# Performance work log

Measured on AMD Instinct MI355X. Metric: run time of the kernel, lower is better.

## Reference

```python
import jax, jax.numpy as jnp
import numpy as np

NSAMPLE = 32
LAMBDA = 0.5


def setup_inputs() -> dict:
    key = jax.random.key(0)
    k1, k2, k3, k4, k5 = jax.random.split(key, 5)
    B, N, NPOINT, C, NCOMP = 4, 8192, 2048, 64, 16
    xyz = jax.random.normal(k1, (B, N, 3), dtype=jnp.float32)
    new_xyz = jax.random.normal(k2, (B, NPOINT, 3), dtype=jnp.float32)
    components = jax.random.randint(k3, (B, N, 1), 0, NCOMP, dtype=jnp.int64)
    new_components = jax.random.randint(k4, (B, NPOINT, 1), 0, NCOMP, dtype=jnp.int64)
    features = jax.random.normal(k5, (B, C, N), dtype=jnp.float32)
    return {"xyz": xyz, "new_xyz": new_xyz, "components": components,
            "new_components": new_components, "features": features}


def _gag_knn(new_xyz, xyz, new_comp, comp, k, lam):
    # squared pairwise distances (B, npoint, N), same math as sum((src-dst)**2)
    diff = new_xyz[:, :, None, :] - xyz[:, None, :, :]
    dists = jnp.sum(diff * diff, axis=-1)
    # component-aware rescale
    mask = comp[:, None, :] == new_comp[:, :, None]  # (B, npoint, N)
    dists = jnp.where(mask, dists * lam, dists * (1.0 - lam))
    # full argsort then take first k (faithful to original)
    idx = jnp.argsort(dists, axis=-1)[:, :, :k]  # (B, npoint, k)
    return idx.astype(jnp.int32)


def reference(xyz, new_xyz, components, new_components, features):
    comp = components[..., 0]
    new_comp = new_components[..., 0]
    idx = _gag_knn(new_xyz, xyz, new_comp, comp, NSAMPLE, LAMBDA)  # (B, npoint, ns)

    # group xyz: gather along N -> (B, npoint, ns, 3)
    grouped_xyz = jnp.take_along_axis(xyz[:, None, :, :], idx[..., None], axis=2)
    grouped_xyz = grouped_xyz - new_xyz[:, :, None, :]
    grouped_xyz = jnp.transpose(grouped_xyz, (0, 3, 1, 2))  # (B, 3, npoint, ns)

    # group features: (B, C, N) -> (B, npoint, ns, C) -> (B, C, npoint, ns)
    feats_bnc = jnp.transpose(features, (0, 2, 1))  # (B, N, C)
    grouped_feats = jnp.take_along_axis(feats_bnc[:, None, :, :], idx[..., None], axis=2)
    grouped_feats = jnp.transpose(grouped_feats, (0, 3, 1, 2))  # (B, C, npoint, ns)

    return jnp.concatenate([grouped_xyz, grouped_feats], axis=1)  # (B, 3+C, npoint, ns)
```

## Files before the change

kernel.cpp:

```cpp
#include <hip/hip_runtime.h>


#define BQ 4
#define NN_ 8192
#define NPOINT 2048
#define CF 64
#define NS 32
#define T1 256
#define PER (NN_ / T1)
#define QB 8
#define CAPQ 192
#define M_EPS 1e-3f

#define KNN_BLOCKS (BQ * NPOINT / QB)
#define TR_BLOCKS  ((NN_ / 32) * (CF / 32) * BQ)

#define SMEM_BYTES (QB * T1 * 4 + QB * CAPQ * 8 + QB * 4 + QB * 4)

__device__ __forceinline__ float rfl(float x) {
  return __int_as_float(__builtin_amdgcn_readfirstlane(__float_as_int(x)));
}

__global__ __launch_bounds__(256) void knn_tr_kernel(
    const float* __restrict__ xyz, const float* __restrict__ new_xyz,
    const float* __restrict__ features, int* __restrict__ idxOut,
    float* __restrict__ featsT) {
  __shared__ __align__(16) char smem[SMEM_BYTES];
  const int tid = threadIdx.x;

  if (blockIdx.x >= KNN_BLOCKS) {
    float(*tr)[33] = (float(*)[33])smem;
    const int t = blockIdx.x - KNN_BLOCKS;
    const int n0 = (t & 255) * 32;
    const int c0 = ((t >> 8) & 1) * 32;
    const int b = t >> 9;
    const int tx = tid & 31;
    const int ty = tid >> 5;
#pragma unroll
    for (int i = 0; i < 4; i++) {
      int c = c0 + ty + i * 8;
      tr[ty + i * 8][tx] = features[(size_t)b * CF * NN_ + (size_t)c * NN_ + n0 + tx];
    }
    __syncthreads();
#pragma unroll
    for (int i = 0; i < 4; i++) {
      int nrow = n0 + ty + i * 8;
      featsT[(size_t)b * NN_ * CF + (size_t)nrow * CF + c0 + tx] = tr[tx][ty + i * 8];
    }
    return;
  }

  float(*sMin)[T1] = (float(*)[T1])smem;
  unsigned long long(*cand)[CAPQ] =
      (unsigned long long(*)[CAPQ])(smem + QB * T1 * 4);
  float* sTheta = (float*)(smem + QB * T1 * 4 + QB * CAPQ * 8);
  int* cnt = (int*)(smem + QB * T1 * 4 + QB * CAPQ * 8 + QB * 4);

  const int tile = blockIdx.x;
  const int b = tile / (NPOINT / QB);
  const int q0 = b * NPOINT + (tile % (NPOINT / QB)) * QB;
  const int lane = tid & 63;
  const int wid = tid >> 6;

  float qx2[QB], qy2[QB], qz2[QB], qnn[QB];
#pragma unroll
  for (int k = 0; k < QB; k++) {
    float ax = new_xyz[(q0 + k) * 3 + 0];
    float ay = new_xyz[(q0 + k) * 3 + 1];
    float az = new_xyz[(q0 + k) * 3 + 2];
    qx2[k] = rfl(-2.0f * ax);
    qy2[k] = rfl(-2.0f * ay);
    qz2[k] = rfl(-2.0f * az);
    qnn[k] = rfl(ax * ax + ay * ay + az * az);
  }

  const float4* __restrict__ base4 = (const float4*)(xyz + (size_t)b * NN_ * 3);

  float smin_r[QB];
#pragma unroll
  for (int k = 0; k < QB; k++) smin_r[k] = 3.4e38f;

#pragma unroll
  for (int g = 0; g < PER / 4; g++) {
    const int v = g * 768 + tid * 3;
    float4 v0 = base4[v + 0];
    float4 v1 = base4[v + 1];
    float4 v2 = base4[v + 2];
    float xs[4] = {v0.x, v0.w, v1.z, v2.y};
    float ys[4] = {v0.y, v1.x, v1.w, v2.z};
    float zs[4] = {v0.z, v1.y, v2.x, v2.w};
#pragma unroll
    for (int i = 0; i < 4; i++) {
      float pp = fmaf(zs[i], zs[i], fmaf(ys[i], ys[i], xs[i] * xs[i]));
#pragma unroll
      for (int k = 0; k < QB; k++) {
        float t = fmaf(xs[i], qx2[k], pp);
        t = fmaf(ys[i], qy2[k], t);
        t = fmaf(zs[i], qz2[k], t);
        smin_r[k] = fminf(smin_r[k], t);
      }
    }
  }

#pragma unroll
  for (int k = 0; k < QB; k++) sMin[k][tid] = smin_r[k];
  if (tid < QB) cnt[tid] = 0;
  __syncthreads();

#pragma unroll
  for (int t2 = 0; t2 < 2; t2++) {
    const int k = wid * 2 + t2;
    float m = fminf(fminf(sMin[k][lane], sMin[k][lane + 64]),
                    fminf(sMin[k][lane + 128], sMin[k][lane + 192]));
#pragma unroll
    for (int kk = 2; kk <= 64; kk <<= 1) {
#pragma unroll
      for (int jj = kk >> 1; jj > 0; jj >>= 1) {
        float o = __shfl_xor(m, jj);
        bool up = ((lane & kk) == 0);
        bool lower = ((lane & jj) == 0);
        m = (up == lower) ? fminf(m, o) : fmaxf(m, o);
      }
    }
    if (lane == 31) sTheta[k] = m + qnn[k] + M_EPS;
  }
  __syncthreads();

  float thd[QB], th2[QB];
#pragma unroll
  for (int k = 0; k < QB; k++) {
    thd[k] = rfl(sTheta[k]);
    th2[k] = rfl(thd[k] + M_EPS - qnn[k]);
  }

#pragma unroll
  for (int g = 0; g < PER / 4; g++) {
    const int v = g * 768 + tid * 3;
    float4 v0 = base4[v + 0];
    float4 v1 = base4[v + 1];
    float4 v2 = base4[v + 2];
    float xs[4] = {v0.x, v0.w, v1.z, v2.y};
    float ys[4] = {v0.y, v1.x, v1.w, v2.z};
    float zs[4] = {v0.z, v1.y, v2.x, v2.w};
#pragma unroll
    for (int i = 0; i < 4; i++) {
      float pp = fmaf(zs[i], zs[i], fmaf(ys[i], ys[i], xs[i] * xs[i]));
#pragma unroll
      for (int k = 0; k < QB; k++) {
        float t = fmaf(xs[i], qx2[k], pp);
        t = fmaf(ys[i], qy2[k], t);
        t = fmaf(zs[i], qz2[k], t);
        if (t <= th2[k]) {
          float dx = xs[i] - (-0.5f * qx2[k]);
          float dy = ys[i] - (-0.5f * qy2[k]);
          float dz = zs[i] - (-0.5f * qz2[k]);
          float d = __fadd_rn(__fadd_rn(__fmul_rn(dx, dx), __fmul_rn(dy, dy)),
                              __fmul_rn(dz, dz));
          if (d <= thd[k]) {
            int n = g * 1024 + tid * 4 + i;
            int pos = atomicAdd(&cnt[k], 1);
            if (pos < CAPQ)
              cand[k][pos] =
                  ((unsigned long long)__float_as_uint(d) << 32) | (unsigned)n;
          }
        }
      }
    }
  }
  __syncthreads();

#pragma unroll
  for (int t2 = 0; t2 < 2; t2++) {
    const int k = wid * 2 + t2;
    const int m = cnt[k] < CAPQ ? cnt[k] : CAPQ;
    for (int i = lane; i < m; i += 64) {
      unsigned long long x = cand[k][i];
      int r = 0;
      for (int j = 0; j < m; j++) r += (cand[k][j] < x) ? 1 : 0;
      if (r < NS) idxOut[(q0 + k) * NS + r] = (int)(x & 0xffffffffu);
    }
  }
}

#define FSTR 68
__global__ __launch_bounds__(256) void group_kernel(const float* __restrict__ xyz,
                                                    const float* __restrict__ new_xyz,
                                                    const float* __restrict__ featsT,
                                                    const int* __restrict__ idxArr,
                                                    float* __restrict__ out) {
  const int q = blockIdx.x;
  const int b = q / NPOINT;
  const int p = q - b * NPOINT;
  const int tid = threadIdx.x;

  __shared__ int sIdx[NS];
  __shared__ __align__(16) float ldsF[NS * FSTR];
  __shared__ float ldsX[3 * NS];

  if (tid < NS) sIdx[tid] = idxArr[q * NS + tid];
  __syncthreads();

  {
    int s = tid >> 3, r = tid & 7;
    int nn = sIdx[s];
    const float4* src = (const float4*)(featsT + ((size_t)b * NN_ + nn) * CF);
    float4 v0 = src[r * 2];
    float4 v1 = src[r * 2 + 1];
    float4* dst = (float4*)(ldsF + s * FSTR + r * 8);
    dst[0] = v0;
    dst[1] = v1;
  }
  if (tid < 96) {
    int dd = tid >> 5, s = tid & 31;
    int nn = sIdx[s];
    ldsX[dd * NS + s] = xyz[((size_t)b * NN_ + nn) * 3 + dd] -
                        new_xyz[(size_t)q * 3 + dd];
  }
  __syncthreads();

  const int s = tid & 31;
  const int r0 = tid >> 5;
#pragma unroll
  for (int k = 0; k < 9; k++) {
    int row = r0 + k * 8;
    if (row < 67) {
      float v = (row < 3) ? ldsX[row * NS + s] : ldsF[s * FSTR + (row - 3)];
      out[(((size_t)b * 67 + row) * NPOINT + p) * NS + s] = v;
    }
  }
}

extern "C" void kernel_launch(void* const* d_in, const int* in_sizes, int n_in,
                              void* d_out, int out_size, void* d_ws, size_t ws_size,
                              hipStream_t stream) {
  const float* xyz      = (const float*)d_in[0];
  const float* new_xyz  = (const float*)d_in[1];
  const float* features = (const float*)d_in[4];
  float* out = (float*)d_out;

  int* idxArr = (int*)d_ws;
  float* featsT = (float*)((char*)d_ws + (size_t)BQ * NPOINT * NS * sizeof(int));

  knn_tr_kernel<<<KNN_BLOCKS + TR_BLOCKS, T1, 0, stream>>>(xyz, new_xyz, features,
                                                           idxArr, featsT);
  group_kernel<<<BQ * NPOINT, T1, 0, stream>>>(xyz, new_xyz, featsT, idxArr, out);
}
```

Baseline: 134.0 us.

## Defer exact distance to rank phase and shrink candidate buffers in LDS

The candidate-collection pass no longer computes the exact rounded distance and only appends point indices for those passing the expanded threshold. The exact distances are computed afterwards from global xyz, then packed keys are staged into LDS reusing the sMin region. CAPQ is reduced from 192 to 128, which cuts LDS per block, and the loops are less aggressively unrolled, so more blocks fit per CU with lower register pressure. The risks are a weaker filter (more candidates, possible overflow past 128), the extra global gathers, and the added __syncthreads inside a loop indexed per wave.

```diff
diff --git a/kernel.cpp b/kernel.cpp
--- a/kernel.cpp
+++ b/kernel.cpp
@@ -9,13 +9,15 @@
 #define T1 256
 #define PER (NN_ / T1)
 #define QB 8
-#define CAPQ 192
+#define CAPQ 128
 #define M_EPS 1e-3f
 
 #define KNN_BLOCKS (BQ * NPOINT / QB)
 #define TR_BLOCKS  ((NN_ / 32) * (CF / 32) * BQ)
 
-#define SMEM_BYTES (QB * T1 * 4 + QB * CAPQ * 8 + QB * 4 + QB * 4)
+#define REG_A (QB * T1 * 4)
+#define REG_B (QB * CAPQ * 4)
+#define SMEM_BYTES (REG_A + REG_B + QB * 4 + QB * 4)
 
 __device__ __forceinline__ float rfl(float x) {
   return __int_as_float(__builtin_amdgcn_readfirstlane(__float_as_int(x)));
@@ -51,10 +53,10 @@
   }
 
   float(*sMin)[T1] = (float(*)[T1])smem;
-  unsigned long long(*cand)[CAPQ] =
-      (unsigned long long(*)[CAPQ])(smem + QB * T1 * 4);
-  float* sTheta = (float*)(smem + QB * T1 * 4 + QB * CAPQ * 8);
-  int* cnt = (int*)(smem + QB * T1 * 4 + QB * CAPQ * 8 + QB * 4);
+  unsigned long long(*keys)[CAPQ] = (unsigned long long(*)[CAPQ])smem;
+  unsigned int(*candI)[CAPQ] = (unsigned int(*)[CAPQ])(smem + REG_A);
+  float* sTheta = (float*)(smem + REG_A + REG_B);
+  int* cnt = (int*)(smem + REG_A + REG_B + QB * 4);
 
   const int tile = blockIdx.x;
   const int b = tile / (NPOINT / QB);
@@ -80,7 +82,7 @@
 #pragma unroll
   for (int k = 0; k < QB; k++) smin_r[k] = 3.4e38f;
 
-#pragma unroll
+#pragma unroll 2
   for (int g = 0; g < PER / 4; g++) {
     const int v = g * 768 + tid * 3;
     float4 v0 = base4[v + 0];
@@ -126,14 +128,12 @@
   }
   __syncthreads();
 
-  float thd[QB], th2[QB];
-#pragma unroll
-  for (int k = 0; k < QB; k++) {
-    thd[k] = rfl(sTheta[k]);
-    th2[k] = rfl(thd[k] + M_EPS - qnn[k]);
-  }
-
-#pragma unroll
+  float th2[QB];
+#pragma unroll
+  for (int k = 0; k < QB; k++)
+    th2[k] = rfl(sTheta[k] + M_EPS - qnn[k]);
+
+#pragma unroll 1
   for (int g = 0; g < PER / 4; g++) {
     const int v = g * 768 + tid * 3;
     float4 v0 = base4[v + 0];
@@ -145,40 +145,63 @@
 #pragma unroll
     for (int i = 0; i < 4; i++) {
       float pp = fmaf(zs[i], zs[i], fmaf(ys[i], ys[i], xs[i] * xs[i]));
+      const int n = g * 1024 + tid * 4 + i;
 #pragma unroll
       for (int k = 0; k < QB; k++) {
         float t = fmaf(xs[i], qx2[k], pp);
         t = fmaf(ys[i], qy2[k], t);
         t = fmaf(zs[i], qz2[k], t);
         if (t <= th2[k]) {
-          float dx = xs[i] - (-0.5f * qx2[k]);
-          float dy = ys[i] - (-0.5f * qy2[k]);
-          float dz = zs[i] - (-0.5f * qz2[k]);
-          float d = __fadd_rn(__fadd_rn(__fmul_rn(dx, dx), __fmul_rn(dy, dy)),
-                              __fmul_rn(dz, dz));
-          if (d <= thd[k]) {
-            int n = g * 1024 + tid * 4 + i;
-            int pos = atomicAdd(&cnt[k], 1);
-            if (pos < CAPQ)
-              cand[k][pos] =
-                  ((unsigned long long)__float_as_uint(d) << 32) | (unsigned)n;
-          }
+          int pos = atomicAdd(&cnt[k], 1);
+          if (pos < CAPQ) candI[k][pos] = (unsigned)n;
         }
       }
     }
   }
   __syncthreads();
 
+  const float* __restrict__ baseF = xyz + (size_t)b * NN_ * 3;
 #pragma unroll
   for (int t2 = 0; t2 < 2; t2++) {
     const int k = wid * 2 + t2;
+    const int qq = q0 + k;
     const int m = cnt[k] < CAPQ ? cnt[k] : CAPQ;
-    for (int i = lane; i < m; i += 64) {
-      unsigned long long x = cand[k][i];
-      int r = 0;
-      for (int j = 0; j < m; j++) r += (cand[k][j] < x) ? 1 : 0;
-      if (r < NS) idxOut[(q0 + k) * NS + r] = (int)(x & 0xffffffffu);
-    }
+    const float qxk = new_xyz[qq * 3 + 0];
+    const float qyk = new_xyz[qq * 3 + 1];
+    const float qzk = new_xyz[qq * 3 + 2];
+
+    unsigned long long keyreg[CAPQ / 64];
+#pragma unroll
+    for (int c = 0; c < CAPQ / 64; c++) {
+      const int i = lane + c * 64;
+      if (i < m) {
+        const int n = (int)candI[k][i];
+        float dx = baseF[n * 3 + 0] - qxk;
+        float dy = baseF[n * 3 + 1] - qyk;
+        float dz = baseF[n * 3 + 2] - qzk;
+        float d = __fadd_rn(__fadd_rn(__fmul_rn(dx, dx), __fmul_rn(dy, dy)),
+                            __fmul_rn(dz, dz));
+        keyreg[c] = ((unsigned long long)__float_as_uint(d) << 32) | (unsigned)n;
+      }
+    }
+    __syncthreads();
+#pragma unroll
+    for (int c = 0; c < CAPQ / 64; c++) {
+      const int i = lane + c * 64;
+      if (i < m) keys[k][i] = keyreg[c];
+    }
+    __syncthreads();
+#pragma unroll
+    for (int c = 0; c < CAPQ / 64; c++) {
+      const int i = lane + c * 64;
+      if (i < m) {
+        unsigned long long x = keys[k][i];
+        int r = 0;
+        for (int j = 0; j < m; j++) r += (keys[k][j] < x) ? 1 : 0;
+        if (r < NS) idxOut[qq * NS + r] = (int)(x & 0xffffffffu);
+      }
+    }
+    __syncthreads();
   }
 }
 
```

Measured after the change: 129.3 us, median of 2. -3.5%, faster.
